# Kernel optimization log

Hardware: AMD Instinct MI355X
Metric: run time of the kernel (lower is better)

## Reference

```python
import jax, jax.numpy as jnp
import numpy as np

N_NODES = 100000
N_EDGES = 1600000
IN_FEATS, HIDDEN, N_CLASSES = 128, 64, 16


def gcn_layer(x, src, dst, W, b, n_nodes):
    # DGL GraphConv, norm='both': h = D_in^{-1/2} A (D_out^{-1/2} x) W + b
    # (W applied before aggregation since in_feats > out_feats, as DGL does)
    ones = jnp.ones((src.shape[0],), dtype=x.dtype)
    deg_out = jax.ops.segment_sum(ones, src, num_segments=n_nodes)
    deg_in = jax.ops.segment_sum(ones, dst, num_segments=n_nodes)
    norm_src = jax.lax.rsqrt(jnp.clip(deg_out, 1.0))  # [N]
    norm_dst = jax.lax.rsqrt(jnp.clip(deg_in, 1.0))   # [N]
    h = (x * norm_src[:, None]) @ W                    # [N, out]
    msgs = h[src]                                      # [E, out] gather
    agg = jax.ops.segment_sum(msgs, dst, num_segments=n_nodes)  # [N, out]
    return agg * norm_dst[:, None] + b


def setup_inputs() -> dict:
    key = jax.random.key(0)
    k1, k2, k3, k4, k5, k6, k7 = jax.random.split(key, 7)
    x = jax.random.normal(k1, (N_NODES, IN_FEATS), dtype=jnp.float32)
    src = jax.random.randint(k2, (N_EDGES,), 0, N_NODES, dtype=jnp.int32)
    dst = jax.random.randint(k3, (N_EDGES,), 0, N_NODES, dtype=jnp.int32)
    s1 = 1.0 / np.sqrt(IN_FEATS)
    s2 = 1.0 / np.sqrt(HIDDEN)
    W1 = jax.random.uniform(k4, (IN_FEATS, HIDDEN), jnp.float32, -s1, s1)
    b1 = jnp.zeros((HIDDEN,), dtype=jnp.float32)
    W2 = jax.random.uniform(k5, (HIDDEN, N_CLASSES), jnp.float32, -s2, s2)
    b2 = jnp.zeros((N_CLASSES,), dtype=jnp.float32)
    return {"x": x, "src": src, "dst": dst, "W1": W1, "b1": b1, "W2": W2, "b2": b2}


def reference(x, src, dst, W1, b1, W2, b2):
    h = gcn_layer(x, src, dst, W1, b1, N_NODES)
    h = jax.nn.relu(h)
    h = gcn_layer(h, src, dst, W2, b2, N_NODES)
    return jax.nn.softmax(h, axis=-1)  # [N, num_classes]
```

## Files before the change

### kernel.cpp

```cpp
#include <hip/hip_runtime.h>
#include <hip/hip_fp16.h>
#include <math.h>


constexpr int N_NODES = 100000;
constexpr int N_EDGES = 1600000;
constexpr int IN_F    = 128;
constexpr int HID     = 64;
constexpr int NC      = 16;

constexpr int NB_D   = 391;
constexpr int STR    = 4608;
constexpr int NBLK_P = 256;
constexpr int EPB    = N_EDGES / NBLK_P;
constexpr int CAPB   = 64;
constexpr int CSTR   = 16;

typedef _Float16 f16x8 __attribute__((ext_vector_type(8)));
typedef _Float16 f16x4 __attribute__((ext_vector_type(4)));
typedef float    f32x4 __attribute__((ext_vector_type(4)));

__global__ __launch_bounds__(512) void k_init(int* __restrict__ cursD,
                                              int* __restrict__ cursS) {
    int t = threadIdx.x;
    if (t < NB_D) {
        cursD[t * CSTR] = t * STR;
        cursS[t * CSTR] = t * STR;
    }
}

__global__ __launch_bounds__(1024) void k_part(const int* __restrict__ src,
                                               const int* __restrict__ dst,
                                               int* __restrict__ cursD,
                                               int* __restrict__ cursS,
                                               unsigned int* __restrict__ ebufD,
                                               unsigned char* __restrict__ ebufS) {
    __shared__ unsigned int  bufD[NB_D * CAPB];
    __shared__ unsigned char bufS[NB_D * CAPB];
    __shared__ int cD[NB_D], cS[NB_D], baseD[NB_D], baseS[NB_D];
    const int t = threadIdx.x, b = blockIdx.x;
    for (int i = t; i < NB_D; i += 1024) { cD[i] = 0; cS[i] = 0; }
    __syncthreads();
    const int beg = b * EPB, end = beg + EPB;
    for (int i = beg + t; i < end; i += 1024) {
        int d = dst[i], s = src[i];
        int bD = d >> 8;
        int c  = atomicAdd(&cD[bD], 1);
        if (c < CAPB) bufD[(bD << 6) + c] = ((unsigned)(d & 255) << 17) | (unsigned)s;
        int bS = s >> 8;
        int c2 = atomicAdd(&cS[bS], 1);
        if (c2 < CAPB) bufS[(bS << 6) + c2] = (unsigned char)(s & 255);
    }
    __syncthreads();
    for (int i = t; i < NB_D; i += 1024) {
        int c = min(cD[i], CAPB);
        cD[i] = c;
        baseD[i] = atomicAdd(&cursD[i * CSTR], c);
        int c2 = min(cS[i], CAPB);
        cS[i] = c2;
        baseS[i] = atomicAdd(&cursS[i * CSTR], c2);
    }
    __syncthreads();
    for (int slot = t; slot < NB_D * CAPB; slot += 1024) {
        int bk = slot >> 6, idx = slot & 63;
        if (idx < cD[bk]) ebufD[baseD[bk] + idx] = bufD[slot];
    }
    for (int slot = t; slot < NB_D * CAPB; slot += 1024) {
        int bk = slot >> 6, idx = slot & 63;
        if (idx < cS[bk]) ebufS[baseS[bk] + idx] = bufS[slot];
    }
}

__global__ __launch_bounds__(256) void k_bmergeS(const int* __restrict__ cursS,
                                                 const unsigned char* __restrict__ ebufS,
                                                 float* __restrict__ norm_src) {
    __shared__ int cnt[256];
    const int t = threadIdx.x, b = blockIdx.x;
    const int beg = b * STR;
    int end = cursS[b * CSTR];
    if (end > beg + STR) end = beg + STR;
    cnt[t] = 0;
    __syncthreads();
    for (int i = beg + t; i < end; i += 256)
        atomicAdd(&cnt[ebufS[i]], 1);
    __syncthreads();
    int node = b * 256 + t;
    if (node < N_NODES)
        norm_src[node] = 1.0f / sqrtf(fmaxf((float)cnt[t], 1.0f));
}

constexpr int PADK = 136;
__global__ __launch_bounds__(256) void k_gemm1(
        const float* __restrict__ x, const float* __restrict__ W1,
        const float* __restrict__ norm_src, __half* __restrict__ h1h) {
    __shared__ _Float16 xh[64 * PADK];
    __shared__ _Float16 wt[64 * PADK];
    const int t = threadIdx.x;
    const int row0 = blockIdx.x * 64;
    for (int i = t; i < 64 * 32; i += 256) {
        int c4 = i & 31, rr = i >> 5;
        int gr = row0 + rr;
        float4 v = (gr < N_NODES) ? *(const float4*)&x[(size_t)gr * IN_F + c4 * 4]
                                  : float4{0.f, 0.f, 0.f, 0.f};
        f16x4 hv;
        hv[0] = (_Float16)v.x; hv[1] = (_Float16)v.y;
        hv[2] = (_Float16)v.z; hv[3] = (_Float16)v.w;
        *(f16x4*)&xh[rr * PADK + c4 * 4] = hv;
    }
    for (int i = t; i < 64 * 32; i += 256) {
        int n = i & 63, kq = i >> 6;
        int k0 = kq * 4;
        f16x4 hv;
        #pragma unroll
        for (int j = 0; j < 4; ++j)
            hv[j] = (_Float16)W1[(size_t)(k0 + j) * HID + n];
        *(f16x4*)&wt[n * PADK + k0] = hv;
    }
    __syncthreads();
    const int w = t >> 6;
    const int l = t & 63;
    const int m = l & 15, q = l >> 4;
    f32x4 acc0 = {0,0,0,0}, acc1 = {0,0,0,0}, acc2 = {0,0,0,0}, acc3 = {0,0,0,0};
    #pragma unroll
    for (int kc = 0; kc < 4; ++kc) {
        f16x8 af = *(const f16x8*)&xh[(16 * w + m) * PADK + kc * 32 + q * 8];
        f16x8 b0 = *(const f16x8*)&wt[( 0 + m) * PADK + kc * 32 + q * 8];
        f16x8 b1 = *(const f16x8*)&wt[(16 + m) * PADK + kc * 32 + q * 8];
        f16x8 b2 = *(const f16x8*)&wt[(32 + m) * PADK + kc * 32 + q * 8];
        f16x8 b3 = *(const f16x8*)&wt[(48 + m) * PADK + kc * 32 + q * 8];
        acc0 = __builtin_amdgcn_mfma_f32_16x16x32_f16(af, b0, acc0, 0, 0, 0);
        acc1 = __builtin_amdgcn_mfma_f32_16x16x32_f16(af, b1, acc1, 0, 0, 0);
        acc2 = __builtin_amdgcn_mfma_f32_16x16x32_f16(af, b2, acc2, 0, 0, 0);
        acc3 = __builtin_amdgcn_mfma_f32_16x16x32_f16(af, b3, acc3, 0, 0, 0);
    }
    _Float16* out = (_Float16*)h1h;
    #pragma unroll
    for (int r = 0; r < 4; ++r) {
        int row_g = row0 + 16 * w + q * 4 + r;
        if (row_g < N_NODES) {
            float ns = norm_src[row_g];
            size_t base = (size_t)row_g * HID + m;
            out[base +  0] = (_Float16)(acc0[r] * ns);
            out[base + 16] = (_Float16)(acc1[r] * ns);
            out[base + 32] = (_Float16)(acc2[r] * ns);
            out[base + 48] = (_Float16)(acc3[r] * ns);
        }
    }
}

__global__ __launch_bounds__(1024) void k_agg1(
        const int* __restrict__ cursD, const unsigned int* __restrict__ ebufD,
        const __half* __restrict__ h1h, const float* __restrict__ ns,
        const float* __restrict__ b1, const float* __restrict__ W2,
        __half* __restrict__ h2h) {
    __shared__ unsigned int ebl[STR];
    __shared__ int csr_l[STR];
    __shared__ float rb[128 * 68];
    __shared__ float W2t[16 * 68];
    __shared__ int cnt[256], curs[256], rs_l[256], wsum[4];
    const int t = threadIdx.x, b = blockIdx.x;
    const int beg = b * STR;
    int total = cursD[b * CSTR] - beg;
    if (total > STR) total = STR;
    const int nv = total >> 2;
    const uint4* s4 = (const uint4*)(ebufD + beg);
    for (int i = t; i < nv; i += 1024) ((uint4*)ebl)[i] = s4[i];
    for (int i = (nv << 2) + t; i < total; i += 1024) ebl[i] = ebufD[beg + i];
    if (t < 256) cnt[t] = 0;
    for (int i = t; i < HID * NC; i += 1024) {
        int k = i >> 4, c = i & 15;
        W2t[c * 68 + k] = W2[i];
    }
    __syncthreads();
    for (int i = t; i < total; i += 1024)
        atomicAdd(&cnt[ebl[i] >> 17], 1);
    __syncthreads();
    int x = 0, v = 0;
    const int lane = t & 63, wid = t >> 6;
    if (t < 256) {
        x = cnt[t]; v = x;
        #pragma unroll
        for (int d = 1; d < 64; d <<= 1) { int u = __shfl_up(v, d, 64); if (lane >= d) v += u; }
        if (lane == 63) wsum[wid] = v;
    }
    __syncthreads();
    if (t < 256) {
        int woff = 0;
        for (int ww = 0; ww < wid; ++ww) woff += wsum[ww];
        int rs = woff + v - x;
        rs_l[t] = rs;
        curs[t] = rs;
    }
    __syncthreads();
    for (int i = t; i < total; i += 1024) {
        unsigned int e = ebl[i];
        int pos = atomicAdd(&curs[e >> 17], 1);
        csr_l[pos] = (int)(e & 0x1FFFFu);
    }
    __syncthreads();
    const int w = t >> 6, l = t & 63, g = l >> 3, j = l & 7;
    const float4 bb0 = *(const float4*)&b1[j * 8 + 0];
    const float4 bb1 = *(const float4*)&b1[j * 8 + 4];
    #pragma unroll
    for (int pp = 0; pp < 2; ++pp) {
        const int nl = pp * 128 + w * 8 + g;
        const int pbeg = rs_l[nl], deg = cnt[nl];
        const int pend = pbeg + deg;
        float a0=0,a1=0,a2=0,a3=0,a4=0,a5=0,a6=0,a7=0;
        int p = pbeg;
        for (; p + 8 <= pend; p += 8) {
            float4 g4[8];
            #pragma unroll
            for (int u = 0; u < 8; ++u) {
                int s = csr_l[p + u];
                g4[u] = *(const float4*)&h1h[(size_t)s * HID + j * 8];
            }
            #pragma unroll
            for (int u = 0; u < 8; ++u) {
                const __half2* hh = (const __half2*)&g4[u];
                float2 f0 = __half22float2(hh[0]);
                float2 f1 = __half22float2(hh[1]);
                float2 f2 = __half22float2(hh[2]);
                float2 f3 = __half22float2(hh[3]);
                a0 += f0.x; a1 += f0.y; a2 += f1.x; a3 += f1.y;
                a4 += f2.x; a5 += f2.y; a6 += f3.x; a7 += f3.y;
            }
        }
        for (; p < pend; ++p) {
            int s = csr_l[p];
            float4 g4 = *(const float4*)&h1h[(size_t)s * HID + j * 8];
            const __half2* hh = (const __half2*)&g4;
            float2 f0 = __half22float2(hh[0]);
            float2 f1 = __half22float2(hh[1]);
            float2 f2 = __half22float2(hh[2]);
            float2 f3 = __half22float2(hh[3]);
            a0 += f0.x; a1 += f0.y; a2 += f1.x; a3 += f1.y;
            a4 += f2.x; a5 += f2.y; a6 += f3.x; a7 += f3.y;
        }
        const float n = 1.0f / sqrtf(fmaxf((float)deg, 1.0f));
        float4 v0, v1;
        v0.x = fmaxf(a0 * n + bb0.x, 0.f);
        v0.y = fmaxf(a1 * n + bb0.y, 0.f);
        v0.z = fmaxf(a2 * n + bb0.z, 0.f);
        v0.w = fmaxf(a3 * n + bb0.w, 0.f);
        v1.x = fmaxf(a4 * n + bb1.x, 0.f);
        v1.y = fmaxf(a5 * n + bb1.y, 0.f);
        v1.z = fmaxf(a6 * n + bb1.z, 0.f);
        v1.w = fmaxf(a7 * n + bb1.w, 0.f);
        const int rrow = w * 8 + g;
        *(float4*)&rb[rrow * 68 + j * 8 + 0] = v0;
        *(float4*)&rb[rrow * 68 + j * 8 + 4] = v1;
        float o0 = 0.f, o1 = 0.f;
        #pragma unroll
        for (int k4 = 0; k4 < 16; ++k4) {
            float4 r  = *(float4*)&rb[rrow * 68 + k4 * 4];
            float4 wa = *(float4*)&W2t[j * 68 + k4 * 4];
            float4 wb = *(float4*)&W2t[(j + 8) * 68 + k4 * 4];
            o0 += r.x * wa.x + r.y * wa.y + r.z * wa.z + r.w * wa.w;
            o1 += r.x * wb.x + r.y * wb.y + r.z * wb.z + r.w * wb.w;
        }
        const int node = b * 256 + nl;
        if (node < N_NODES) {
            const float nsv = ns[node];
            _Float16* o = (_Float16*)h2h;
            o[(size_t)node * NC + j]     = (_Float16)(o0 * nsv);
            o[(size_t)node * NC + j + 8] = (_Float16)(o1 * nsv);
        }
    }
}

__global__ __launch_bounds__(1024) void k_agg2(
        const int* __restrict__ cursD, const unsigned int* __restrict__ ebufD,
        const __half* __restrict__ h2h, const float* __restrict__ b2,
        float* __restrict__ out) {
    __shared__ unsigned int ebl[STR];
    __shared__ int csr_l[STR];
    __shared__ int cnt[256], curs[256], rs_l[256], wsum[4];
    const int t = threadIdx.x, b = blockIdx.x;
    const int beg = b * STR;
    int total = cursD[b * CSTR] - beg;
    if (total > STR) total = STR;
    const int nv = total >> 2;
    const uint4* s4 = (const uint4*)(ebufD + beg);
    for (int i = t; i < nv; i += 1024) ((uint4*)ebl)[i] = s4[i];
    for (int i = (nv << 2) + t; i < total; i += 1024) ebl[i] = ebufD[beg + i];
    if (t < 256) cnt[t] = 0;
    __syncthreads();
    for (int i = t; i < total; i += 1024)
        atomicAdd(&cnt[ebl[i] >> 17], 1);
    __syncthreads();
    int x = 0, v = 0;
    const int lane = t & 63, wid = t >> 6;
    if (t < 256) {
        x = cnt[t]; v = x;
        #pragma unroll
        for (int d = 1; d < 64; d <<= 1) { int u = __shfl_up(v, d, 64); if (lane >= d) v += u; }
        if (lane == 63) wsum[wid] = v;
    }
    __syncthreads();
    if (t < 256) {
        int woff = 0;
        for (int ww = 0; ww < wid; ++ww) woff += wsum[ww];
        int rs = woff + v - x;
        rs_l[t] = rs;
        curs[t] = rs;
    }
    __syncthreads();
    for (int i = t; i < total; i += 1024) {
        unsigned int e = ebl[i];
        int pos = atomicAdd(&curs[e >> 17], 1);
        csr_l[pos] = (int)(e & 0x1FFFFu);
    }
    __syncthreads();
    const int w = t >> 6, l = t & 63, g = l >> 2, sub = l & 3;
    const int nl = w * 16 + g;
    const int pbeg = rs_l[nl], deg = cnt[nl];
    const int pend = pbeg + deg;
    float acc[4] = {0, 0, 0, 0};
    int p = pbeg;
    for (; p + 8 <= pend; p += 8) {
        float2 g8[8];
        #pragma unroll
        for (int u = 0; u < 8; ++u) {
            int s = csr_l[p + u];
            g8[u] = *(const float2*)&h2h[(size_t)s * NC + sub * 4];
        }
        #pragma unroll
        for (int u = 0; u < 8; ++u) {
            const __half2* hh = (const __half2*)&g8[u];
            float2 f0 = __half22float2(hh[0]);
            float2 f1 = __half22float2(hh[1]);
            acc[0] += f0.x; acc[1] += f0.y; acc[2] += f1.x; acc[3] += f1.y;
        }
    }
    for (; p < pend; ++p) {
        int s = csr_l[p];
        float2 g2 = *(const float2*)&h2h[(size_t)s * NC + sub * 4];
        const __half2* hh = (const __half2*)&g2;
        float2 f0 = __half22float2(hh[0]);
        float2 f1 = __half22float2(hh[1]);
        acc[0] += f0.x; acc[1] += f0.y; acc[2] += f1.x; acc[3] += f1.y;
    }
    const float n = 1.0f / sqrtf(fmaxf((float)deg, 1.0f));
    const float4 bv = *(const float4*)&b2[sub * 4];
    float vv[4];
    vv[0] = acc[0] * n + bv.x;
    vv[1] = acc[1] * n + bv.y;
    vv[2] = acc[2] * n + bv.z;
    vv[3] = acc[3] * n + bv.w;
    float m = fmaxf(fmaxf(vv[0], vv[1]), fmaxf(vv[2], vv[3]));
    m = fmaxf(m, __shfl_xor(m, 1, 4));
    m = fmaxf(m, __shfl_xor(m, 2, 4));
    float e0 = __expf(vv[0] - m), e1 = __expf(vv[1] - m);
    float e2 = __expf(vv[2] - m), e3 = __expf(vv[3] - m);
    float s = e0 + e1 + e2 + e3;
    s += __shfl_xor(s, 1, 4);
    s += __shfl_xor(s, 2, 4);
    const float inv = 1.0f / s;
    const int node = b * 256 + nl;
    if (node < N_NODES) {
        float4 o4 = { e0 * inv, e1 * inv, e2 * inv, e3 * inv };
        *(float4*)&out[(size_t)node * NC + sub * 4] = o4;
    }
}

extern "C" void kernel_launch(void* const* d_in, const int* in_sizes, int n_in,
                              void* d_out, int out_size, void* d_ws, size_t ws_size,
                              hipStream_t stream) {
    const float* x   = (const float*)d_in[0];
    const int*   src = (const int*)  d_in[1];
    const int*   dst = (const int*)  d_in[2];
    const float* W1  = (const float*)d_in[3];
    const float* b1  = (const float*)d_in[4];
    const float* W2  = (const float*)d_in[5];
    const float* b2  = (const float*)d_in[6];
    float* out = (float*)d_out;

    const size_t N = N_NODES;
    float* ws       = (float*)d_ws;
    int*   wsI      = (int*)d_ws;
    float* norm_src = ws;
    __half* h1h     = (__half*)(ws + 2 * N);
    __half* h2h     = (__half*)(ws + 34 * N);
    unsigned int*  ebufD = (unsigned int*)(wsI + 66 * N);
    unsigned char* ebufS = (unsigned char*)(wsI + 66 * N + NB_D * STR);
    int*   cursD    = wsI + 132 * N;
    int*   cursS    = wsI + 132 * N + 8192;

    k_init<<<1, 512, 0, stream>>>(cursD, cursS);
    k_part<<<NBLK_P, 1024, 0, stream>>>(src, dst, cursD, cursS, ebufD, ebufS);
    k_bmergeS<<<NB_D, 256, 0, stream>>>(cursS, ebufS, norm_src);
    k_gemm1<<<(N_NODES + 63) / 64, 256, 0, stream>>>(x, W1, norm_src, h1h);
    k_agg1<<<NB_D, 1024, 0, stream>>>(cursD, ebufD, h1h, norm_src, b1, W2, h2h);
    k_agg2<<<NB_D, 1024, 0, stream>>>(cursD, ebufD, h2h, b2, out);
}
```

Baseline: 198.5 us.

## Count source degrees with global atomics and halve destination bucket size

Drops the source-side bucket partition and the k_bmergeS kernel. Out-degrees are now counted with global atomicAdd directly in k_part, and the normalization is computed inline where it is used. Destination buckets shrink from 256 to 128 nodes (782 blocks of 512 threads), which gives more, smaller aggregation blocks with less LDS each and likely better occupancy. The trade is 1.6M global atomics on random addresses in exchange for one fewer kernel launch and less shared-memory staging. The smaller per-block capacity (CAPB 32, STR 2432) also raises the risk of overflowing a bucket.

```diff
diff --git a/kernel.cpp b/kernel.cpp
--- a/kernel.cpp
+++ b/kernel.cpp
@@ -9,90 +9,59 @@
 constexpr int HID     = 64;
 constexpr int NC      = 16;
 
-constexpr int NB_D   = 391;
-constexpr int STR    = 4608;
+constexpr int NB_D   = 782;
+constexpr int STR    = 2432;
 constexpr int NBLK_P = 256;
 constexpr int EPB    = N_EDGES / NBLK_P;
-constexpr int CAPB   = 64;
+constexpr int CAPB   = 32;
 constexpr int CSTR   = 16;
 
 typedef _Float16 f16x8 __attribute__((ext_vector_type(8)));
 typedef _Float16 f16x4 __attribute__((ext_vector_type(4)));
 typedef float    f32x4 __attribute__((ext_vector_type(4)));
 
-__global__ __launch_bounds__(512) void k_init(int* __restrict__ cursD,
-                                              int* __restrict__ cursS) {
-    int t = threadIdx.x;
-    if (t < NB_D) {
-        cursD[t * CSTR] = t * STR;
-        cursS[t * CSTR] = t * STR;
-    }
+__global__ __launch_bounds__(1024) void k_init(int* __restrict__ deg_src,
+                                               int* __restrict__ cursD) {
+    int i = blockIdx.x * 1024 + threadIdx.x;
+    if (i < N_NODES) deg_src[i] = 0;
+    if (blockIdx.x == 0 && threadIdx.x < NB_D) cursD[threadIdx.x * CSTR] = threadIdx.x * STR;
 }
 
 __global__ __launch_bounds__(1024) void k_part(const int* __restrict__ src,
                                                const int* __restrict__ dst,
                                                int* __restrict__ cursD,
-                                               int* __restrict__ cursS,
                                                unsigned int* __restrict__ ebufD,
-                                               unsigned char* __restrict__ ebufS) {
-    __shared__ unsigned int  bufD[NB_D * CAPB];
-    __shared__ unsigned char bufS[NB_D * CAPB];
-    __shared__ int cD[NB_D], cS[NB_D], baseD[NB_D], baseS[NB_D];
+                                               int* __restrict__ deg_src) {
+    __shared__ unsigned int bufD[NB_D * CAPB];
+    __shared__ int cD[NB_D], baseD[NB_D];
     const int t = threadIdx.x, b = blockIdx.x;
-    for (int i = t; i < NB_D; i += 1024) { cD[i] = 0; cS[i] = 0; }
+    for (int i = t; i < NB_D; i += 1024) cD[i] = 0;
     __syncthreads();
     const int beg = b * EPB, end = beg + EPB;
     for (int i = beg + t; i < end; i += 1024) {
         int d = dst[i], s = src[i];
-        int bD = d >> 8;
+        atomicAdd(&deg_src[s], 1);
+        int bD = d >> 7;
         int c  = atomicAdd(&cD[bD], 1);
-        if (c < CAPB) bufD[(bD << 6) + c] = ((unsigned)(d & 255) << 17) | (unsigned)s;
-        int bS = s >> 8;
-        int c2 = atomicAdd(&cS[bS], 1);
-        if (c2 < CAPB) bufS[(bS << 6) + c2] = (unsigned char)(s & 255);
+        if (c < CAPB) bufD[(bD << 5) + c] = ((unsigned)(d & 127) << 17) | (unsigned)s;
     }
     __syncthreads();
     for (int i = t; i < NB_D; i += 1024) {
         int c = min(cD[i], CAPB);
         cD[i] = c;
         baseD[i] = atomicAdd(&cursD[i * CSTR], c);
-        int c2 = min(cS[i], CAPB);
-        cS[i] = c2;
-        baseS[i] = atomicAdd(&cursS[i * CSTR], c2);
     }
     __syncthreads();
     for (int slot = t; slot < NB_D * CAPB; slot += 1024) {
-        int bk = slot >> 6, idx = slot & 63;
+        int bk = slot >> 5, idx = slot & 31;
         if (idx < cD[bk]) ebufD[baseD[bk] + idx] = bufD[slot];
     }
-    for (int slot = t; slot < NB_D * CAPB; slot += 1024) {
-        int bk = slot >> 6, idx = slot & 63;
-        if (idx < cS[bk]) ebufS[baseS[bk] + idx] = bufS[slot];
-    }
-}
-
-__global__ __launch_bounds__(256) void k_bmergeS(const int* __restrict__ cursS,
-                                                 const unsigned char* __restrict__ ebufS,
-                                                 float* __restrict__ norm_src) {
-    __shared__ int cnt[256];
-    const int t = threadIdx.x, b = blockIdx.x;
-    const int beg = b * STR;
-    int end = cursS[b * CSTR];
-    if (end > beg + STR) end = beg + STR;
-    cnt[t] = 0;
-    __syncthreads();
-    for (int i = beg + t; i < end; i += 256)
-        atomicAdd(&cnt[ebufS[i]], 1);
-    __syncthreads();
-    int node = b * 256 + t;
-    if (node < N_NODES)
-        norm_src[node] = 1.0f / sqrtf(fmaxf((float)cnt[t], 1.0f));
 }
 
 constexpr int PADK = 136;
 __global__ __launch_bounds__(256) void k_gemm1(
         const float* __restrict__ x, const float* __restrict__ W1,
-        const float* __restrict__ norm_src, __half* __restrict__ h1h) {
+        const int* __restrict__ deg_src, __half* __restrict__ h1h) {
     __shared__ _Float16 xh[64 * PADK];
     __shared__ _Float16 wt[64 * PADK];
     const int t = threadIdx.x;
@@ -138,7 +107,7 @@
     for (int r = 0; r < 4; ++r) {
         int row_g = row0 + 16 * w + q * 4 + r;
         if (row_g < N_NODES) {
-            float ns = norm_src[row_g];
+            float ns = 1.0f / sqrtf(fmaxf((float)deg_src[row_g], 1.0f));
             size_t base = (size_t)row_g * HID + m;
             out[base +  0] = (_Float16)(acc0[r] * ns);
             out[base + 16] = (_Float16)(acc1[r] * ns);
@@ -148,51 +117,50 @@
     }
 }
 
-__global__ __launch_bounds__(1024) void k_agg1(
+__global__ __launch_bounds__(512) void k_agg1(
         const int* __restrict__ cursD, const unsigned int* __restrict__ ebufD,
-        const __half* __restrict__ h1h, const float* __restrict__ ns,
+        const __half* __restrict__ h1h, const int* __restrict__ deg_src,
         const float* __restrict__ b1, const float* __restrict__ W2,
         __half* __restrict__ h2h) {
     __shared__ unsigned int ebl[STR];
     __shared__ int csr_l[STR];
-    __shared__ float rb[128 * 68];
+    __shared__ float rb[64 * 68];
     __shared__ float W2t[16 * 68];
-    __shared__ int cnt[256], curs[256], rs_l[256], wsum[4];
+    __shared__ int cnt[128], curs[128], rs_l[128], wsum[2];
     const int t = threadIdx.x, b = blockIdx.x;
     const int beg = b * STR;
     int total = cursD[b * CSTR] - beg;
     if (total > STR) total = STR;
     const int nv = total >> 2;
     const uint4* s4 = (const uint4*)(ebufD + beg);
-    for (int i = t; i < nv; i += 1024) ((uint4*)ebl)[i] = s4[i];
-    for (int i = (nv << 2) + t; i < total; i += 1024) ebl[i] = ebufD[beg + i];
-    if (t < 256) cnt[t] = 0;
-    for (int i = t; i < HID * NC; i += 1024) {
+    for (int i = t; i < nv; i += 512) ((uint4*)ebl)[i] = s4[i];
+    for (int i = (nv << 2) + t; i < total; i += 512) ebl[i] = ebufD[beg + i];
+    if (t < 128) cnt[t] = 0;
+    for (int i = t; i < HID * NC; i += 512) {
         int k = i >> 4, c = i & 15;
         W2t[c * 68 + k] = W2[i];
     }
     __syncthreads();
-    for (int i = t; i < total; i += 1024)
+    for (int i = t; i < total; i += 512)
         atomicAdd(&cnt[ebl[i] >> 17], 1);
     __syncthreads();
     int x = 0, v = 0;
     const int lane = t & 63, wid = t >> 6;
-    if (t < 256) {
+    if (t < 128) {
         x = cnt[t]; v = x;
         #pragma unroll
         for (int d = 1; d < 64; d <<= 1) { int u = __shfl_up(v, d, 64); if (lane >= d) v += u; }
         if (lane == 63) wsum[wid] = v;
     }
     __syncthreads();
-    if (t < 256) {
-        int woff = 0;
-        for (int ww = 0; ww < wid; ++ww) woff += wsum[ww];
+    if (t < 128) {
+        int woff = (wid == 1) ? wsum[0] : 0;
         int rs = woff + v - x;
         rs_l[t] = rs;
         curs[t] = rs;
     }
     __syncthreads();
-    for (int i = t; i < total; i += 1024) {
+    for (int i = t; i < total; i += 512) {
         unsigned int e = ebl[i];
         int pos = atomicAdd(&curs[e >> 17], 1);
         csr_l[pos] = (int)(e & 0x1FFFFu);
@@ -203,7 +171,7 @@
     const float4 bb1 = *(const float4*)&b1[j * 8 + 4];
     #pragma unroll
     for (int pp = 0; pp < 2; ++pp) {
-        const int nl = pp * 128 + w * 8 + g;
+        const int nl = pp * 64 + w * 8 + g;
         const int pbeg = rs_l[nl], deg = cnt[nl];
         const int pend = pbeg + deg;
         float a0=0,a1=0,a2=0,a3=0,a4=0,a5=0,a6=0,a7=0;
@@ -259,9 +227,9 @@
             o0 += r.x * wa.x + r.y * wa.y + r.z * wa.z + r.w * wa.w;
             o1 += r.x * wb.x + r.y * wb.y + r.z * wb.z + r.w * wb.w;
         }
-        const int node = b * 256 + nl;
+        const int node = b * 128 + nl;
         if (node < N_NODES) {
-            const float nsv = ns[node];
+            const float nsv = 1.0f / sqrtf(fmaxf((float)deg_src[node], 1.0f));
             _Float16* o = (_Float16*)h2h;
             o[(size_t)node * NC + j]     = (_Float16)(o0 * nsv);
             o[(size_t)node * NC + j + 8] = (_Float16)(o1 * nsv);
@@ -269,44 +237,43 @@
     }
 }
 
-__global__ __launch_bounds__(1024) void k_agg2(
+__global__ __launch_bounds__(512) void k_agg2(
         const int* __restrict__ cursD, const unsigned int* __restrict__ ebufD,
         const __half* __restrict__ h2h, const float* __restrict__ b2,
         float* __restrict__ out) {
     __shared__ unsigned int ebl[STR];
     __shared__ int csr_l[STR];
-    __shared__ int cnt[256], curs[256], rs_l[256], wsum[4];
+    __shared__ int cnt[128], curs[128], rs_l[128], wsum[2];
     const int t = threadIdx.x, b = blockIdx.x;
     const int beg = b * STR;
     int total = cursD[b * CSTR] - beg;
     if (total > STR) total = STR;
     const int nv = total >> 2;
     const uint4* s4 = (const uint4*)(ebufD + beg);
-    for (int i = t; i < nv; i += 1024) ((uint4*)ebl)[i] = s4[i];
-    for (int i = (nv << 2) + t; i < total; i += 1024) ebl[i] = ebufD[beg + i];
-    if (t < 256) cnt[t] = 0;
-    __syncthreads();
-    for (int i = t; i < total; i += 1024)
+    for (int i = t; i < nv; i += 512) ((uint4*)ebl)[i] = s4[i];
+    for (int i = (nv << 2) + t; i < total; i += 512) ebl[i] = ebufD[beg + i];
+    if (t < 128) cnt[t] = 0;
+    __syncthreads();
+    for (int i = t; i < total; i += 512)
         atomicAdd(&cnt[ebl[i] >> 17], 1);
     __syncthreads();
     int x = 0, v = 0;
     const int lane = t & 63, wid = t >> 6;
-    if (t < 256) {
+    if (t < 128) {
         x = cnt[t]; v = x;
         #pragma unroll
         for (int d = 1; d < 64; d <<= 1) { int u = __shfl_up(v, d, 64); if (lane >= d) v += u; }
         if (lane == 63) wsum[wid] = v;
     }
     __syncthreads();
-    if (t < 256) {
-        int woff = 0;
-        for (int ww = 0; ww < wid; ++ww) woff += wsum[ww];
+    if (t < 128) {
+        int woff = (wid == 1) ? wsum[0] : 0;
         int rs = woff + v - x;
         rs_l[t] = rs;
         curs[t] = rs;
     }
     __syncthreads();
-    for (int i = t; i < total; i += 1024) {
+    for (int i = t; i < total; i += 512) {
         unsigned int e = ebl[i];
         int pos = atomicAdd(&curs[e >> 17], 1);
         csr_l[pos] = (int)(e & 0x1FFFFu);
@@ -357,7 +324,7 @@
     s += __shfl_xor(s, 1, 4);
     s += __shfl_xor(s, 2, 4);
     const float inv = 1.0f / s;
-    const int node = b * 256 + nl;
+    const int node = b * 128 + nl;
     if (node < N_NODES) {
         float4 o4 = { e0 * inv, e1 * inv, e2 * inv, e3 * inv };
         *(float4*)&out[(size_t)node * NC + sub * 4] = o4;
@@ -377,20 +344,17 @@
     float* out = (float*)d_out;
 
     const size_t N = N_NODES;
+    int*   wsI      = (int*)d_ws;
     float* ws       = (float*)d_ws;
-    int*   wsI      = (int*)d_ws;
-    float* norm_src = ws;
+    int*   deg_src  = wsI;
     __half* h1h     = (__half*)(ws + 2 * N);
     __half* h2h     = (__half*)(ws + 34 * N);
-    unsigned int*  ebufD = (unsigned int*)(wsI + 66 * N);
-    unsigned char* ebufS = (unsigned char*)(wsI + 66 * N + NB_D * STR);
+    unsigned int* ebufD = (unsigned int*)(wsI + 66 * N);
     int*   cursD    = wsI + 132 * N;
-    int*   cursS    = wsI + 132 * N + 8192;
-
-    k_init<<<1, 512, 0, stream>>>(cursD, cursS);
-    k_part<<<NBLK_P, 1024, 0, stream>>>(src, dst, cursD, cursS, ebufD, ebufS);
-    k_bmergeS<<<NB_D, 256, 0, stream>>>(cursS, ebufS, norm_src);
-    k_gemm1<<<(N_NODES + 63) / 64, 256, 0, stream>>>(x, W1, norm_src, h1h);
-    k_agg1<<<NB_D, 1024, 0, stream>>>(cursD, ebufD, h1h, norm_src, b1, W2, h2h);
-    k_agg2<<<NB_D, 1024, 0, stream>>>(cursD, ebufD, h2h, b2, out);
-}
+
+    k_init<<<(N_NODES + 1023) / 1024, 1024, 0, stream>>>(deg_src, cursD);
+    k_part<<<NBLK_P, 1024, 0, stream>>>(src, dst, cursD, ebufD, deg_src);
+    k_gemm1<<<(N_NODES + 63) / 64, 256, 0, stream>>>(x, W1, deg_src, h1h);
+    k_agg1<<<NB_D, 512, 0, stream>>>(cursD, ebufD, h1h, deg_src, b1, W2, h2h);
+    k_agg2<<<NB_D, 512, 0, stream>>>(cursD, ebufD, h2h, b2, out);
+}
```

Result: slower. 246.6 us (+24.2%).
